# Optimization experiments

Hardware: AMD Instinct MI355X
Metric: run time of the kernel (lower is better)

The kernel has to match this reference:

```python
import jax, jax.numpy as jnp
import numpy as np

WINDOW = 100   # window_size
HEADS = 8      # num_heads
KDIM = 64      # Keras MHA key_dim (= value_dim by default)
D = 512        # model dim (query/key/value feature dim)
B = 8
L = 4096       # not a multiple of WINDOW -> pad_len = 4


def setup_inputs() -> dict:
    key = jax.random.key(0)
    ks = jax.random.split(key, 5)
    s = 0.02  # small init scale like glorot
    return {
        "x":  jax.random.normal(ks[0], (B, L, D), jnp.float32),
        "Wq": jax.random.normal(ks[1], (D, HEADS, KDIM), jnp.float32) * s,
        "bq": jnp.zeros((HEADS, KDIM), jnp.float32),
        "Wk": jax.random.normal(ks[2], (D, HEADS, KDIM), jnp.float32) * s,
        "bk": jnp.zeros((HEADS, KDIM), jnp.float32),
        "Wv": jax.random.normal(ks[3], (D, HEADS, KDIM), jnp.float32) * s,
        "bv": jnp.zeros((HEADS, KDIM), jnp.float32),
        "Wo": jax.random.normal(ks[4], (HEADS, KDIM, D), jnp.float32) * s,
        "bo": jnp.zeros((D,), jnp.float32),
    }


def reference(x, Wq, bq, Wk, bk, Wv, bv, Wo, bo):
    Bx, Lx, Dx = x.shape
    pad_len = (WINDOW - Lx % WINDOW) % WINDOW
    xp = jnp.pad(x, ((0, 0), (0, pad_len), (0, 0)))          # [B, L+pad, D]
    n_win = (Lx + pad_len) // WINDOW
    xw = xp.reshape(Bx * n_win, WINDOW, Dx)                  # [B*N, W, D]

    # Keras MultiHeadAttention(num_heads=HEADS, key_dim=KDIM), self-attention
    q = jnp.einsum('bwd,dhk->bwhk', xw, Wq) + bq             # [B*N, W, H, K]
    k = jnp.einsum('bwd,dhk->bwhk', xw, Wk) + bk
    v = jnp.einsum('bwd,dhk->bwhk', xw, Wv) + bv

    scale = 1.0 / np.sqrt(KDIM).astype(np.float32)
    scores = jnp.einsum('bqhk,bshk->bhqs', q, k) * scale     # [B*N, H, W, W]
    attn = jax.nn.softmax(scores, axis=-1)
    o = jnp.einsum('bhqs,bshk->bqhk', attn, v)               # [B*N, W, H, K]
    y = jnp.einsum('bqhk,hkd->bqd', o, Wo) + bo              # [B*N, W, D]

    return y.reshape(Bx, n_win, WINDOW, Dx)                  # pad_len is static (=4 here)
```

## Files before the change

### kernel.cpp

```cpp
#include <hip/hip_runtime.h>

typedef unsigned short u16;
typedef __attribute__((ext_vector_type(4))) float f32x4;
typedef __attribute__((ext_vector_type(8))) short short8;

#define WIN_SZ 100
#define NWIN 41
#define NBATCH 8
#define SEQ 4096
#define DM 512
#define NHEAD 8
#define KD 64
#define NWINS (NBATCH * NWIN)
#define MROWS (NWINS * WIN_SZ)
#define MBLKS 257
#define TOKPB (NWIN * WIN_SZ)
#define NQKV 1536

#define OFF_XBF   0u
#define OFF_OBUF  16793600u
#define OFF_WQKVT 33587200u
#define OFF_WOT   34373632u
#define OFF_ZBLK  34635776u
#define OFF_BIAS  34636032u
#define OFF_BIAS2 34639104u

__device__ __forceinline__ u16 f2bf(float f) {
  union { float f; unsigned i; } v; v.f = f;
  unsigned r = (v.i + 0x7fffu + ((v.i >> 16) & 1u)) >> 16;
  return (u16)r;
}

__device__ __forceinline__ void gl2lds16(const void* g, void* lds) {
  __builtin_amdgcn_global_load_lds(
      (const __attribute__((address_space(1))) void*)g,
      (__attribute__((address_space(3))) void*)lds, 16, 0, 0);
}

__global__ void prep_k(const float* __restrict__ Wq, const float* __restrict__ Wk,
                       const float* __restrict__ Wv, const float* __restrict__ Wo,
                       const float* __restrict__ bq, const float* __restrict__ bk,
                       const float* __restrict__ bv, const float* __restrict__ bo,
                       u16* __restrict__ ws) {
  __shared__ u16 tile[64][65];
  const int z = blockIdx.z;
  const float* src = (z == 0) ? Wq : (z == 1) ? Wk : (z == 2) ? Wv : Wo;
  u16* dst = (z < 3) ? (ws + OFF_WQKVT + (unsigned)z * 512u * 512u)
                     : (ws + OFF_WOT);
  const int k0 = blockIdx.y * 64, n0 = blockIdx.x * 64;
  const int t = threadIdx.x;
  const int c = t & 63, r4 = t >> 6;
#pragma unroll
  for (int p = 0; p < 16; ++p) {
    int r = p * 4 + r4;
    tile[r][c] = f2bf(src[(size_t)(k0 + r) * 512 + n0 + c]);
  }
  __syncthreads();
#pragma unroll
  for (int p = 0; p < 16; ++p) {
    int r = p * 4 + r4;
    dst[(size_t)(n0 + r) * 512 + k0 + c] = tile[c][r];
  }
  if (blockIdx.x == 0 && blockIdx.y == 0) {
    float* biasF = (float*)(ws + OFF_BIAS);
    float* biasO = (float*)(ws + OFF_BIAS2);
    for (int j = t; j < 512; j += 256) {
      if (z == 0) biasF[j] = bq[j];
      else if (z == 1) biasF[512 + j] = bk[j];
      else if (z == 2) biasF[1024 + j] = bv[j];
      else biasO[j] = bo[j];
    }
    if (z == 3 && t < 128) ws[OFF_ZBLK + t] = 0;
  }
}

__global__ void convx_k(const float* __restrict__ x, u16* __restrict__ ws) {
  u16* xbf = ws + OFF_XBF;
  int i = blockIdx.x * 256 + threadIdx.x;
  if (i >= MROWS * 128) return;
  int m = i >> 7;
  int c4 = (i & 127) * 4;
  int b = m / TOKPB, tk = m - b * TOKPB;
  float4 v = make_float4(0.f, 0.f, 0.f, 0.f);
  if (tk < SEQ) v = *(const float4*)(x + (size_t)(b * SEQ + tk) * DM + c4);
  u16 o[4] = {f2bf(v.x), f2bf(v.y), f2bf(v.z), f2bf(v.w)};
  *(uint2*)(xbf + (size_t)m * DM + c4) = *(const uint2*)o;
}

#define QKS 72
#define PS 136
#define SM_ELEMS 24832

__global__ __launch_bounds__(256, 3)
void qkvattn_k(const u16* __restrict__ ws) {
  __shared__ u16 smem[SM_ELEMS];
  u16* Xs  = smem;
  u16* Wsl = smem + 7168;
  u16* Vt  = smem;
  u16* Qs  = smem + 8704;
  u16* Ks  = smem + 16768;
  u16* P   = smem + 8704;

  const int win = blockIdx.x, h = blockIdx.y;
  const int t = threadIdx.x, w = t >> 6, l = t & 63;
  const int q = l >> 4, cl = l & 15;
  const int lsw = (((t & 7) ^ ((t >> 3) & 7)) * 8);

  unsigned xoff[4];
#pragma unroll
  for (int i = 0; i < 4; ++i) {
    int m = i * 32 + (t >> 3);
    xoff[i] = (m < WIN_SZ)
                  ? (OFF_XBF + (unsigned)(win * WIN_SZ + m) * DM + lsw)
                  : OFF_ZBLK;
  }
  unsigned woff[6];
#pragma unroll
  for (int i = 0; i < 6; ++i) {
    int g = i * 32 + (t >> 3);
    unsigned nrow = (unsigned)(g >> 6) * 512u + (unsigned)h * 64u + (g & 63);
    woff[i] = OFF_WQKVT + nrow * DM + lsw;
  }

  f32x4 acc_p[7][3] = {};
  for (int k0 = 0; k0 < DM; k0 += 64) {
    __syncthreads();
#pragma unroll
    for (int i = 0; i < 4; ++i)
      if (i * 32 + w * 8 < 112)
        gl2lds16(ws + xoff[i] + (xoff[i] == OFF_ZBLK ? 0u : (unsigned)k0),
                 &Xs[(i * 32 + w * 8) * 64]);
#pragma unroll
    for (int i = 0; i < 6; ++i)
      gl2lds16(ws + woff[i] + k0, &Wsl[(i * 32 + w * 8) * 64]);
    __syncthreads();
#pragma unroll
    for (int ks = 0; ks < 2; ++ks) {
      const int ko = ks * 32 + q * 8;
      const int koS = ko ^ ((cl & 7) << 3);
      short8 af[7], bf[3];
#pragma unroll
      for (int mt = 0; mt < 7; ++mt)
        af[mt] = *(const short8*)&Xs[(mt * 16 + cl) * 64 + koS];
#pragma unroll
      for (int ntl = 0; ntl < 3; ++ntl)
        bf[ntl] = *(const short8*)&Wsl[((3 * w + ntl) * 16 + cl) * 64 + koS];
      __builtin_amdgcn_s_setprio(1);
#pragma unroll
      for (int mt = 0; mt < 7; ++mt)
#pragma unroll
        for (int ntl = 0; ntl < 3; ++ntl)
          acc_p[mt][ntl] = __builtin_amdgcn_mfma_f32_16x16x32_bf16(
              af[mt], bf[ntl], acc_p[mt][ntl], 0, 0, 0);
      __builtin_amdgcn_s_setprio(0);
    }
  }
  __syncthreads();

  {
    const float* biasF = (const float*)(ws + OFF_BIAS);
#pragma unroll
    for (int ntl = 0; ntl < 3; ++ntl) {
      const int nt = 3 * w + ntl;
      const int cw = (nt & 3) * 16 + cl;
      const float bb = biasF[(nt >> 2) * 512 + h * 64 + cw];
      if (nt < 8) {
        u16* dst = (nt < 4) ? Qs : Ks;
#pragma unroll
        for (int mt = 0; mt < 7; ++mt)
#pragma unroll
          for (int r = 0; r < 4; ++r) {
            const int tok = mt * 16 + q * 4 + r;
            dst[tok * QKS + cw] = f2bf(acc_p[mt][ntl][r] + bb);
          }
      } else {
#pragma unroll
        for (int mt = 0; mt < 7; ++mt) {
          u16 pk[4];
#pragma unroll
          for (int r = 0; r < 4; ++r) pk[r] = f2bf(acc_p[mt][ntl][r] + bb);
          *(uint2*)&Vt[cw * PS + mt * 16 + q * 4] = *(const uint2*)pk;
        }
      }
    }
    {
      const int row = t >> 2, c4 = (t & 3) * 4;
      *(uint2*)&Vt[row * PS + 112 + c4] = make_uint2(0u, 0u);
    }
  }
  __syncthreads();

  const int nmt = (w < 3) ? 2 : 1;
  const int mt0 = w, mt1 = w + 4;

  f32x4 accs[2][7];
#pragma unroll
  for (int im = 0; im < 2; ++im) {
    if (im < nmt) {
      const int mt = (im == 0) ? mt0 : mt1;
      const int ar = (mt * 16 + cl) * QKS + q * 8;
      short8 a0 = *(const short8*)&Qs[ar];
      short8 a1 = *(const short8*)&Qs[ar + 32];
      __builtin_amdgcn_s_setprio(1);
#pragma unroll
      for (int nt = 0; nt < 7; ++nt) {
        const int br = (nt * 16 + cl) * QKS + q * 8;
        short8 b0 = *(const short8*)&Ks[br];
        short8 b1 = *(const short8*)&Ks[br + 32];
        f32x4 c = {};
        c = __builtin_amdgcn_mfma_f32_16x16x32_bf16(a0, b0, c, 0, 0, 0);
        c = __builtin_amdgcn_mfma_f32_16x16x32_bf16(a1, b1, c, 0, 0, 0);
        accs[im][nt] = c;
      }
      __builtin_amdgcn_s_setprio(0);
    }
  }

  const float scale = 0.125f;
#pragma unroll
  for (int im = 0; im < 2; ++im) {
    if (im < nmt) {
#pragma unroll
      for (int r = 0; r < 4; ++r) {
        float mx = -1e30f;
#pragma unroll
        for (int nt = 0; nt < 7; ++nt) {
          float s = accs[im][nt][r] * scale;
          if ((nt < 6) || (cl < 4)) mx = fmaxf(mx, s);
        }
        mx = fmaxf(mx, __shfl_xor(mx, 1, 64));
        mx = fmaxf(mx, __shfl_xor(mx, 2, 64));
        mx = fmaxf(mx, __shfl_xor(mx, 4, 64));
        mx = fmaxf(mx, __shfl_xor(mx, 8, 64));
        float sum = 0.f;
#pragma unroll
        for (int nt = 0; nt < 7; ++nt) {
          float s = accs[im][nt][r] * scale;
          bool valid = (nt < 6) || (cl < 4);
          float e = valid ? __expf(s - mx) : 0.f;
          accs[im][nt][r] = e;
          sum += e;
        }
        sum += __shfl_xor(sum, 1, 64);
        sum += __shfl_xor(sum, 2, 64);
        sum += __shfl_xor(sum, 4, 64);
        sum += __shfl_xor(sum, 8, 64);
        float inv = 1.0f / sum;
#pragma unroll
        for (int nt = 0; nt < 7; ++nt) accs[im][nt][r] *= inv;
      }
    }
  }
  __syncthreads();

#pragma unroll
  for (int im = 0; im < 2; ++im) {
    if (im < nmt) {
      const int mt = (im == 0) ? mt0 : mt1;
#pragma unroll
      for (int nt = 0; nt < 7; ++nt)
#pragma unroll
        for (int r = 0; r < 4; ++r)
          P[(mt * 16 + q * 4 + r) * PS + nt * 16 + cl] = f2bf(accs[im][nt][r]);
    }
  }
#pragma unroll
  for (int k2 = 0; k2 < 2; ++k2) {
    const int s = k2 * 256 + t;
    if (s < 448) {
      const int row = s >> 2, c4 = (s & 3) * 4;
      *(uint2*)&P[row * PS + 112 + c4] = make_uint2(0u, 0u);
    }
  }
  __syncthreads();

  f32x4 acco[2][4] = {};
#pragma unroll
  for (int ks = 0; ks < 4; ++ks) {
    const int ko = ks * 32 + q * 8;
    short8 a0 = *(const short8*)&P[(mt0 * 16 + cl) * PS + ko];
    short8 a1 = a0;
    if (nmt == 2) a1 = *(const short8*)&P[(mt1 * 16 + cl) * PS + ko];
    __builtin_amdgcn_s_setprio(1);
#pragma unroll
    for (int nt = 0; nt < 4; ++nt) {
      short8 b = *(const short8*)&Vt[(nt * 16 + cl) * PS + ko];
      acco[0][nt] = __builtin_amdgcn_mfma_f32_16x16x32_bf16(a0, b, acco[0][nt], 0, 0, 0);
      if (nmt == 2)
        acco[1][nt] = __builtin_amdgcn_mfma_f32_16x16x32_bf16(a1, b, acco[1][nt], 0, 0, 0);
    }
    __builtin_amdgcn_s_setprio(0);
  }

  u16* obuf = (u16*)(ws + OFF_OBUF);
  const size_t orow0 = (size_t)win * WIN_SZ;
#pragma unroll
  for (int im = 0; im < 2; ++im) {
    if (im < nmt) {
      const int mt = (im == 0) ? mt0 : mt1;
#pragma unroll
      for (int nt = 0; nt < 4; ++nt)
#pragma unroll
        for (int r = 0; r < 4; ++r) {
          int row = mt * 16 + q * 4 + r;
          if (row < WIN_SZ)
            obuf[(orow0 + row) * DM + h * KD + nt * 16 + cl] = f2bf(acco[im][nt][r]);
        }
    }
  }
}

__global__ __launch_bounds__(256, 4)
void gemm_k(const u16* __restrict__ ws, unsigned aoff0, unsigned btoff,
            unsigned biasoff, float* __restrict__ Cout, int Ntot) {
  __shared__ u16 Alds[128 * 64];
  __shared__ u16 Blds[128 * 64];

  const int t = threadIdx.x;
  const int w = t >> 6;
  const int l = t & 63;
  const int nb = blockIdx.x, mb = blockIdx.y;
  const int m0 = mb * 128, n0 = nb * 128;
  const int lr = t >> 3;
  const int lsw = (((t & 7) ^ ((t >> 3) & 7)) * 8);

  unsigned aoff[4], boff[4];
#pragma unroll
  for (int i = 0; i < 4; ++i) {
    int m = m0 + i * 32 + lr;
    aoff[i] = (m < MROWS) ? (aoff0 + (unsigned)m * DM + lsw) : OFF_ZBLK;
    boff[i] = btoff + (unsigned)(n0 + i * 32 + lr) * DM + lsw;
  }

  f32x4 acc[4][4] = {};
  const int wm = (w & 1) * 64;
  const int wn = (w >> 1) * 64;
  const int q = l >> 4, cl = l & 15;

  for (int k0 = 0; k0 < DM; k0 += 64) {
    __syncthreads();
#pragma unroll
    for (int i = 0; i < 4; ++i) {
      gl2lds16(ws + aoff[i] + (aoff[i] == OFF_ZBLK ? 0u : (unsigned)k0),
               &Alds[(i * 32 + w * 8) * 64]);
      gl2lds16(ws + boff[i] + k0, &Blds[(i * 32 + w * 8) * 64]);
    }
    __syncthreads();
#pragma unroll
    for (int ks = 0; ks < 2; ++ks) {
      short8 av[4], bv_[4];
      const int ko = ks * 32 + q * 8;
      const int koS = ko ^ ((cl & 7) << 3);
#pragma unroll
      for (int mi = 0; mi < 4; ++mi)
        av[mi] = *(const short8*)&Alds[(wm + mi * 16 + cl) * 64 + koS];
#pragma unroll
      for (int ni = 0; ni < 4; ++ni)
        bv_[ni] = *(const short8*)&Blds[(wn + ni * 16 + cl) * 64 + koS];
      __builtin_amdgcn_s_setprio(1);
#pragma unroll
      for (int mi = 0; mi < 4; ++mi)
#pragma unroll
        for (int ni = 0; ni < 4; ++ni)
          acc[mi][ni] = __builtin_amdgcn_mfma_f32_16x16x32_bf16(
              av[mi], bv_[ni], acc[mi][ni], 0, 0, 0);
      __builtin_amdgcn_s_setprio(0);
    }
  }

  const float* biasF = (const float*)(ws + biasoff);
#pragma unroll
  for (int mi = 0; mi < 4; ++mi) {
#pragma unroll
    for (int ni = 0; ni < 4; ++ni) {
      int col = n0 + wn + ni * 16 + cl;
      float bb = biasF[col];
#pragma unroll
      for (int r = 0; r < 4; ++r) {
        int row = m0 + wm + mi * 16 + q * 4 + r;
        if (row < MROWS)
          Cout[(size_t)row * Ntot + col] = acc[mi][ni][r] + bb;
      }
    }
  }
}

extern "C" void kernel_launch(void* const* d_in, const int* in_sizes, int n_in,
                              void* d_out, int out_size, void* d_ws, size_t ws_size,
                              hipStream_t stream) {
  const float* x  = (const float*)d_in[0];
  const float* Wq = (const float*)d_in[1];
  const float* bq = (const float*)d_in[2];
  const float* Wk = (const float*)d_in[3];
  const float* bk = (const float*)d_in[4];
  const float* Wv = (const float*)d_in[5];
  const float* bv = (const float*)d_in[6];
  const float* Wo = (const float*)d_in[7];
  const float* bo = (const float*)d_in[8];

  u16* ws = (u16*)d_ws;

  prep_k<<<dim3(8, 8, 4), dim3(256), 0, stream>>>(
      Wq, Wk, Wv, Wo, bq, bk, bv, bo, ws);
  convx_k<<<dim3((MROWS * 128 + 255) / 256), dim3(256), 0, stream>>>(x, ws);
  qkvattn_k<<<dim3(NWINS, NHEAD), dim3(256), 0, stream>>>(ws);
  gemm_k<<<dim3(DM / 128, MBLKS), dim3(256), 0, stream>>>(
      ws, OFF_OBUF, OFF_WOT, OFF_BIAS2, (float*)d_out, DM);
}
```

Measured before the change: 249.0 us.

## Keep softmax probabilities in registers and merge weight prep with x conversion

Result: no change. 247.5 us (-0.6%).

```diff
diff --git a/kernel.cpp b/kernel.cpp
--- a/kernel.cpp
+++ b/kernel.cpp
@@ -3,6 +3,7 @@
 typedef unsigned short u16;
 typedef __attribute__((ext_vector_type(4))) float f32x4;
 typedef __attribute__((ext_vector_type(8))) short short8;
+typedef __attribute__((ext_vector_type(4))) short short4v;
 
 #define WIN_SZ 100
 #define NWIN 41
@@ -16,6 +17,7 @@
 #define MBLKS 257
 #define TOKPB (NWIN * WIN_SZ)
 #define NQKV 1536
+#define CONV_BLKS ((MROWS * 128 + 255) / 256)
 
 #define OFF_XBF   0u
 #define OFF_OBUF  16793600u
@@ -25,6 +27,8 @@
 #define OFF_BIAS  34636032u
 #define OFF_BIAS2 34639104u
 
+#define MFMA16(a, b, c) __builtin_amdgcn_mfma_f32_16x16x16bf16_1k(a, b, c, 0, 0, 0)
+
 __device__ __forceinline__ u16 f2bf(float f) {
   union { float f; unsigned i; } v; v.f = f;
   unsigned r = (v.i + 0x7fffu + ((v.i >> 16) & 1u)) >> 16;
@@ -37,31 +41,46 @@
       (__attribute__((address_space(3))) void*)lds, 16, 0, 0);
 }
 
-__global__ void prep_k(const float* __restrict__ Wq, const float* __restrict__ Wk,
-                       const float* __restrict__ Wv, const float* __restrict__ Wo,
-                       const float* __restrict__ bq, const float* __restrict__ bk,
-                       const float* __restrict__ bv, const float* __restrict__ bo,
-                       u16* __restrict__ ws) {
+__global__ void prepx_k(const float* __restrict__ x,
+                        const float* __restrict__ Wq, const float* __restrict__ Wk,
+                        const float* __restrict__ Wv, const float* __restrict__ Wo,
+                        const float* __restrict__ bq, const float* __restrict__ bk,
+                        const float* __restrict__ bv, const float* __restrict__ bo,
+                        u16* __restrict__ ws) {
   __shared__ u16 tile[64][65];
-  const int z = blockIdx.z;
+  const int t = threadIdx.x;
+  if (blockIdx.x < CONV_BLKS) {
+    u16* xbf = ws + OFF_XBF;
+    int i = blockIdx.x * 256 + t;
+    if (i >= MROWS * 128) return;
+    int m = i >> 7;
+    int c4 = (i & 127) * 4;
+    int b = m / TOKPB, tk = m - b * TOKPB;
+    float4 v = make_float4(0.f, 0.f, 0.f, 0.f);
+    if (tk < SEQ) v = *(const float4*)(x + (size_t)(b * SEQ + tk) * DM + c4);
+    u16 o[4] = {f2bf(v.x), f2bf(v.y), f2bf(v.z), f2bf(v.w)};
+    *(uint2*)(xbf + (size_t)m * DM + c4) = *(const uint2*)o;
+    return;
+  }
+  const int p = blockIdx.x - CONV_BLKS;
+  const int z = p >> 6, by = (p >> 3) & 7, bx = p & 7;
   const float* src = (z == 0) ? Wq : (z == 1) ? Wk : (z == 2) ? Wv : Wo;
   u16* dst = (z < 3) ? (ws + OFF_WQKVT + (unsigned)z * 512u * 512u)
                      : (ws + OFF_WOT);
-  const int k0 = blockIdx.y * 64, n0 = blockIdx.x * 64;
-  const int t = threadIdx.x;
+  const int k0 = by * 64, n0 = bx * 64;
   const int c = t & 63, r4 = t >> 6;
 #pragma unroll
-  for (int p = 0; p < 16; ++p) {
-    int r = p * 4 + r4;
+  for (int pp = 0; pp < 16; ++pp) {
+    int r = pp * 4 + r4;
     tile[r][c] = f2bf(src[(size_t)(k0 + r) * 512 + n0 + c]);
   }
   __syncthreads();
 #pragma unroll
-  for (int p = 0; p < 16; ++p) {
-    int r = p * 4 + r4;
+  for (int pp = 0; pp < 16; ++pp) {
+    int r = pp * 4 + r4;
     dst[(size_t)(n0 + r) * 512 + k0 + c] = tile[c][r];
   }
-  if (blockIdx.x == 0 && blockIdx.y == 0) {
+  if (bx == 0 && by == 0) {
     float* biasF = (float*)(ws + OFF_BIAS);
     float* biasO = (float*)(ws + OFF_BIAS2);
     for (int j = t; j < 512; j += 256) {
@@ -72,19 +91,6 @@
     }
     if (z == 3 && t < 128) ws[OFF_ZBLK + t] = 0;
   }
-}
-
-__global__ void convx_k(const float* __restrict__ x, u16* __restrict__ ws) {
-  u16* xbf = ws + OFF_XBF;
-  int i = blockIdx.x * 256 + threadIdx.x;
-  if (i >= MROWS * 128) return;
-  int m = i >> 7;
-  int c4 = (i & 127) * 4;
-  int b = m / TOKPB, tk = m - b * TOKPB;
-  float4 v = make_float4(0.f, 0.f, 0.f, 0.f);
-  if (tk < SEQ) v = *(const float4*)(x + (size_t)(b * SEQ + tk) * DM + c4);
-  u16 o[4] = {f2bf(v.x), f2bf(v.y), f2bf(v.z), f2bf(v.w)};
-  *(uint2*)(xbf + (size_t)m * DM + c4) = *(const uint2*)o;
 }
 
 #define QKS 72
@@ -99,7 +105,6 @@
   u16* Vt  = smem;
   u16* Qs  = smem + 8704;
   u16* Ks  = smem + 16768;
-  u16* P   = smem + 8704;
 
   const int win = blockIdx.x, h = blockIdx.y;
   const int t = threadIdx.x, w = t >> 6, l = t & 63;
@@ -176,16 +181,12 @@
       } else {
 #pragma unroll
         for (int mt = 0; mt < 7; ++mt) {
-          u16 pk[4];
-#pragma unroll
-          for (int r = 0; r < 4; ++r) pk[r] = f2bf(acc_p[mt][ntl][r] + bb);
-          *(uint2*)&Vt[cw * PS + mt * 16 + q * 4] = *(const uint2*)pk;
+          u16 pkv[4];
+#pragma unroll
+          for (int r = 0; r < 4; ++r) pkv[r] = f2bf(acc_p[mt][ntl][r] + bb);
+          *(uint2*)&Vt[cw * PS + mt * 16 + q * 4] = *(const uint2*)pkv;
         }
       }
-    }
-    {
-      const int row = t >> 2, c4 = (t & 3) * 4;
-      *(uint2*)&Vt[row * PS + 112 + c4] = make_uint2(0u, 0u);
     }
   }
   __syncthreads();
@@ -199,17 +200,17 @@
     if (im < nmt) {
       const int mt = (im == 0) ? mt0 : mt1;
       const int ar = (mt * 16 + cl) * QKS + q * 8;
-      short8 a0 = *(const short8*)&Qs[ar];
-      short8 a1 = *(const short8*)&Qs[ar + 32];
+      short8 qa0 = *(const short8*)&Qs[ar];
+      short8 qa1 = *(const short8*)&Qs[ar + 32];
       __builtin_amdgcn_s_setprio(1);
 #pragma unroll
       for (int nt = 0; nt < 7; ++nt) {
         const int br = (nt * 16 + cl) * QKS + q * 8;
-        short8 b0 = *(const short8*)&Ks[br];
-        short8 b1 = *(const short8*)&Ks[br + 32];
+        short8 kb0 = *(const short8*)&Ks[br];
+        short8 kb1 = *(const short8*)&Ks[br + 32];
         f32x4 c = {};
-        c = __builtin_amdgcn_mfma_f32_16x16x32_bf16(a0, b0, c, 0, 0, 0);
-        c = __builtin_amdgcn_mfma_f32_16x16x32_bf16(a1, b1, c, 0, 0, 0);
+        c = __builtin_amdgcn_mfma_f32_16x16x32_bf16(kb0, qa0, c, 0, 0, 0);
+        c = __builtin_amdgcn_mfma_f32_16x16x32_bf16(kb1, qa1, c, 0, 0, 0);
         accs[im][nt] = c;
       }
       __builtin_amdgcn_s_setprio(0);
@@ -217,95 +218,79 @@
   }
 
   const float scale = 0.125f;
+  unsigned pk[2][7][2];
 #pragma unroll
   for (int im = 0; im < 2; ++im) {
     if (im < nmt) {
-#pragma unroll
-      for (int r = 0; r < 4; ++r) {
-        float mx = -1e30f;
-#pragma unroll
-        for (int nt = 0; nt < 7; ++nt) {
+      float mx = -1e30f;
+#pragma unroll
+      for (int nt = 0; nt < 7; ++nt)
+#pragma unroll
+        for (int r = 0; r < 4; ++r) {
           float s = accs[im][nt][r] * scale;
-          if ((nt < 6) || (cl < 4)) mx = fmaxf(mx, s);
+          accs[im][nt][r] = s;
+          if ((nt < 6) || (q == 0)) mx = fmaxf(mx, s);
         }
-        mx = fmaxf(mx, __shfl_xor(mx, 1, 64));
-        mx = fmaxf(mx, __shfl_xor(mx, 2, 64));
-        mx = fmaxf(mx, __shfl_xor(mx, 4, 64));
-        mx = fmaxf(mx, __shfl_xor(mx, 8, 64));
-        float sum = 0.f;
-#pragma unroll
-        for (int nt = 0; nt < 7; ++nt) {
-          float s = accs[im][nt][r] * scale;
-          bool valid = (nt < 6) || (cl < 4);
-          float e = valid ? __expf(s - mx) : 0.f;
+      mx = fmaxf(mx, __shfl_xor(mx, 16, 64));
+      mx = fmaxf(mx, __shfl_xor(mx, 32, 64));
+      float sum = 0.f;
+#pragma unroll
+      for (int nt = 0; nt < 7; ++nt)
+#pragma unroll
+        for (int r = 0; r < 4; ++r) {
+          bool valid = (nt < 6) || (q == 0);
+          float e = valid ? __expf(accs[im][nt][r] - mx) : 0.f;
           accs[im][nt][r] = e;
           sum += e;
         }
-        sum += __shfl_xor(sum, 1, 64);
-        sum += __shfl_xor(sum, 2, 64);
-        sum += __shfl_xor(sum, 4, 64);
-        sum += __shfl_xor(sum, 8, 64);
-        float inv = 1.0f / sum;
-#pragma unroll
-        for (int nt = 0; nt < 7; ++nt) accs[im][nt][r] *= inv;
-      }
-    }
-  }
-  __syncthreads();
-
+      sum += __shfl_xor(sum, 16, 64);
+      sum += __shfl_xor(sum, 32, 64);
+      float inv = 1.0f / sum;
+#pragma unroll
+      for (int nt = 0; nt < 7; ++nt) {
+        pk[im][nt][0] = (unsigned)f2bf(accs[im][nt][0] * inv) |
+                        ((unsigned)f2bf(accs[im][nt][1] * inv) << 16);
+        pk[im][nt][1] = (unsigned)f2bf(accs[im][nt][2] * inv) |
+                        ((unsigned)f2bf(accs[im][nt][3] * inv) << 16);
+      }
+    }
+  }
+
+  f32x4 acco[2][4] = {};
+  __builtin_amdgcn_s_setprio(1);
+#pragma unroll
+  for (int vt = 0; vt < 4; ++vt) {
+#pragma unroll
+    for (int nt = 0; nt < 7; ++nt) {
+      short4v av = *(const short4v*)&Vt[(vt * 16 + cl) * PS + nt * 16 + q * 4];
+      union { unsigned u[2]; short4v s; } b0, b1;
+      b0.u[0] = pk[0][nt][0]; b0.u[1] = pk[0][nt][1];
+      acco[0][vt] = MFMA16(av, b0.s, acco[0][vt]);
+      if (nmt == 2) {
+        b1.u[0] = pk[1][nt][0]; b1.u[1] = pk[1][nt][1];
+        acco[1][vt] = MFMA16(av, b1.s, acco[1][vt]);
+      }
+    }
+  }
+  __builtin_amdgcn_s_setprio(0);
+
+  u16* obuf = (u16*)(ws + OFF_OBUF);
+  const size_t orow0 = (size_t)win * WIN_SZ;
 #pragma unroll
   for (int im = 0; im < 2; ++im) {
     if (im < nmt) {
       const int mt = (im == 0) ? mt0 : mt1;
-#pragma unroll
-      for (int nt = 0; nt < 7; ++nt)
-#pragma unroll
-        for (int r = 0; r < 4; ++r)
-          P[(mt * 16 + q * 4 + r) * PS + nt * 16 + cl] = f2bf(accs[im][nt][r]);
-    }
-  }
-#pragma unroll
-  for (int k2 = 0; k2 < 2; ++k2) {
-    const int s = k2 * 256 + t;
-    if (s < 448) {
-      const int row = s >> 2, c4 = (s & 3) * 4;
-      *(uint2*)&P[row * PS + 112 + c4] = make_uint2(0u, 0u);
-    }
-  }
-  __syncthreads();
-
-  f32x4 acco[2][4] = {};
-#pragma unroll
-  for (int ks = 0; ks < 4; ++ks) {
-    const int ko = ks * 32 + q * 8;
-    short8 a0 = *(const short8*)&P[(mt0 * 16 + cl) * PS + ko];
-    short8 a1 = a0;
-    if (nmt == 2) a1 = *(const short8*)&P[(mt1 * 16 + cl) * PS + ko];
-    __builtin_amdgcn_s_setprio(1);
-#pragma unroll
-    for (int nt = 0; nt < 4; ++nt) {
-      short8 b = *(const short8*)&Vt[(nt * 16 + cl) * PS + ko];
-      acco[0][nt] = __builtin_amdgcn_mfma_f32_16x16x32_bf16(a0, b, acco[0][nt], 0, 0, 0);
-      if (nmt == 2)
-        acco[1][nt] = __builtin_amdgcn_mfma_f32_16x16x32_bf16(a1, b, acco[1][nt], 0, 0, 0);
-    }
-    __builtin_amdgcn_s_setprio(0);
-  }
-
-  u16* obuf = (u16*)(ws + OFF_OBUF);
-  const size_t orow0 = (size_t)win * WIN_SZ;
-#pragma unroll
-  for (int im = 0; im < 2; ++im) {
-    if (im < nmt) {
-      const int mt = (im == 0) ? mt0 : mt1;
-#pragma unroll
-      for (int nt = 0; nt < 4; ++nt)
-#pragma unroll
-        for (int r = 0; r < 4; ++r) {
-          int row = mt * 16 + q * 4 + r;
-          if (row < WIN_SZ)
-            obuf[(orow0 + row) * DM + h * KD + nt * 16 + cl] = f2bf(acco[im][nt][r]);
+      const int row = mt * 16 + cl;
+      if (row < WIN_SZ) {
+#pragma unroll
+        for (int vt = 0; vt < 4; ++vt) {
+          u16 ov[4];
+#pragma unroll
+          for (int r = 0; r < 4; ++r) ov[r] = f2bf(acco[im][vt][r]);
+          *(uint2*)&obuf[(orow0 + row) * DM + h * KD + vt * 16 + q * 4] =
+              *(const uint2*)ov;
         }
+      }
     }
   }
 }
@@ -400,9 +385,8 @@
 
   u16* ws = (u16*)d_ws;
 
-  prep_k<<<dim3(8, 8, 4), dim3(256), 0, stream>>>(
-      Wq, Wk, Wv, Wo, bq, bk, bv, bo, ws);
-  convx_k<<<dim3((MROWS * 128 + 255) / 256), dim3(256), 0, stream>>>(x, ws);
+  prepx_k<<<dim3(CONV_BLKS + 256), dim3(256), 0, stream>>>(
+      x, Wq, Wk, Wv, Wo, bq, bk, bv, bo, ws);
   qkvattn_k<<<dim3(NWINS, NHEAD), dim3(256), 0, stream>>>(ws);
   gemm_k<<<dim3(DM / 128, MBLKS), dim3(256), 0, stream>>>(
       ws, OFF_OBUF, OFF_WOT, OFF_BIAS2, (float*)d_out, DM);
```
